# Optimization experiments

Measured on AMD Instinct MI355X. Metric: run time of the kernel, lower is better.

Reference implementation:

```python
import jax, jax.numpy as jnp
import numpy as np
from jax import lax

B, T, I, H, L = 64, 512, 256, 512, 2


def setup_inputs() -> dict:
    key = jax.random.key(0)
    ks = jax.random.split(key, 5)
    s_in = (6.0 / (H + I)) ** 0.5   # xavier-uniform-like scale
    s_hh = (6.0 / (H + H)) ** 0.5
    return {
        "x": jax.random.normal(ks[0], (B, T, I), jnp.float32),
        "h_0": jnp.zeros((L, B, H), jnp.float32),
        "W_ih_0": jax.random.normal(ks[1], (H, I), jnp.float32) * s_in,
        "W_hh_0": jax.random.normal(ks[2], (H, H), jnp.float32) * s_hh,
        "b_ih_0": jnp.zeros((H,), jnp.float32),
        "b_hh_0": jnp.zeros((H,), jnp.float32),
        "W_ih_1": jax.random.normal(ks[3], (H, H), jnp.float32) * s_hh,
        "W_hh_1": jax.random.normal(ks[4], (H, H), jnp.float32) * s_hh,
        "b_ih_1": jnp.zeros((H,), jnp.float32),
        "b_hh_1": jnp.zeros((H,), jnp.float32),
    }


def _rnn_layer(xs, h0, W_ih, W_hh, b_ih, b_hh):
    # Precompute the input-to-hidden projection for all timesteps at once
    # (same math as per-step F.linear, just batched): [B,T,H]
    xW = jnp.einsum('bti,hi->bth', xs, W_ih) + b_ih + b_hh

    def step(h, xw_t):  # h:[B,H], xw_t:[B,H]
        h_new = jnp.tanh(xw_t + h @ W_hh.T)
        return h_new, h_new

    h_last, ys = lax.scan(step, h0, jnp.swapaxes(xW, 0, 1))  # ys: [T,B,H]
    return jnp.swapaxes(ys, 0, 1), h_last


def reference(x, h_0, W_ih_0, W_hh_0, b_ih_0, b_hh_0,
              W_ih_1, W_hh_1, b_ih_1, b_hh_1):
    out0, h_n0 = _rnn_layer(x, h_0[0], W_ih_0, W_hh_0, b_ih_0, b_hh_0)
    out1, h_n1 = _rnn_layer(out0, h_0[1], W_ih_1, W_hh_1, b_ih_1, b_hh_1)
    h_n = jnp.stack([h_n0, h_n1], axis=0)  # [L,B,H]
    return out1, h_n
```

## Files before the change

kernel.cpp:

```cpp
#include <hip/hip_runtime.h>


#define kB 64
#define kT 512
#define kI 256
#define kH 512
#define kBH (kB * kH)

typedef _Float16 half8 __attribute__((ext_vector_type(8)));
typedef _Float16 half4v __attribute__((ext_vector_type(4)));
typedef float floatx4 __attribute__((ext_vector_type(4)));

constexpr size_t X16_B   = 0;
constexpr size_t OUT0M_B = 16u * 1024 * 1024;
constexpr size_t H1M_B   = OUT0M_B + (size_t)(kT + 1) * kBH * 2;
constexpr size_t CNT_B   = H1M_B + (size_t)(kT + 1) * kBH * 2;

__device__ inline half8 cvt8(const float* p) {
    const float4* p4 = (const float4*)p;
    float4 a = p4[0], b = p4[1];
    half8 h;
    h[0] = (_Float16)a.x; h[1] = (_Float16)a.y; h[2] = (_Float16)a.z; h[3] = (_Float16)a.w;
    h[4] = (_Float16)b.x; h[5] = (_Float16)b.y; h[6] = (_Float16)b.z; h[7] = (_Float16)b.w;
    return h;
}

__device__ inline void sc_store_half(_Float16* p, _Float16 v) {
    unsigned short u = __builtin_bit_cast(unsigned short, v);
    __hip_atomic_store((unsigned short*)p, u, __ATOMIC_RELAXED, __HIP_MEMORY_SCOPE_AGENT);
}

__device__ inline void wait_flag(const int* p, int target) {
    int guard = 0;
    while (__hip_atomic_load(p, __ATOMIC_RELAXED, __HIP_MEMORY_SCOPE_AGENT) < target) {
        if (++guard > 20000000) break;
    }
    asm volatile("" ::: "memory");
}

__device__ inline void publish(int* p, int lane) {
    asm volatile("" ::: "memory");
    __builtin_amdgcn_s_waitcnt(0x0F70);
    asm volatile("" ::: "memory");
    if (lane == 0)
        __hip_atomic_fetch_add(p, 1, __ATOMIC_RELAXED, __HIP_MEMORY_SCOPE_AGENT);
}

__global__ void cvt_x_kernel(const float* __restrict__ x, _Float16* __restrict__ x16) {
    size_t i = ((size_t)blockIdx.x * blockDim.x + threadIdx.x) * 4;
    size_t stride = (size_t)gridDim.x * blockDim.x * 4;
    const size_t n = (size_t)kB * kT * kI;
    for (; i < n; i += stride) {
        float4 v = *(const float4*)(x + i);
        half4v h;
        h[0] = (_Float16)v.x; h[1] = (_Float16)v.y; h[2] = (_Float16)v.z; h[3] = (_Float16)v.w;
        *(half4v*)(x16 + i) = h;
    }
}

__global__ void setup_kernel(const float* __restrict__ h0, _Float16* __restrict__ out0m,
                             _Float16* __restrict__ h1m, int* __restrict__ cnt) {
    int idx = blockIdx.x * blockDim.x + threadIdx.x;
    if (idx < kBH) out0m[idx] = (_Float16)h0[idx];
    else h1m[idx - kBH] = (_Float16)h0[idx];
    if (idx < 4096) cnt[idx] = 0;
}

__global__ __launch_bounds__(256, 1) void scan_kernel(
    const _Float16* __restrict__ x16, _Float16* __restrict__ out0m,
    _Float16* __restrict__ h1m, int* __restrict__ cnt0, int* __restrict__ cnt1,
    float* __restrict__ out1,
    const float* __restrict__ wih0, const float* __restrict__ whh0,
    const float* __restrict__ bih0, const float* __restrict__ bhh0,
    const float* __restrict__ wih1, const float* __restrict__ whh1,
    const float* __restrict__ bih1, const float* __restrict__ bhh1) {
    __shared__ float lds[2][4][256];

    const int blk = blockIdx.x;
    const int tid = threadIdx.x;
    const int wave = tid >> 6;
    const int lane = tid & 63;
    const int r = lane & 15;
    const int q = lane >> 4;
    const int layer = blk >> 7;
    const int lb = blk & 127;
    const int g = lb >> 5;
    const int ct = lb & 31;
    const int c0 = ct * 16;
    const int b0 = g * 16;

    const int col = lane & 15;
    const int row = wave * 4 + (lane >> 4);
    const int cc = c0 + col;
    const int bb = b0 + row;
    const int roff = (wave * 16 + col) * 4 + (lane >> 4);

    if (layer == 0) {
        half8 wfi[2], wfh[4];
#pragma unroll
        for (int m = 0; m < 2; ++m)
            wfi[m] = cvt8(wih0 + (size_t)(c0 + r) * kI + wave * 64 + m * 32 + q * 8);
#pragma unroll
        for (int m = 0; m < 4; ++m)
            wfh[m] = cvt8(whh0 + (size_t)(c0 + r) * kH + wave * 128 + m * 32 + q * 8);
        const float bias = bih0[cc] + bhh0[cc];
        int* flags = cnt0 + g * kT;

        for (int t = 0; t < kT; ++t) {
            const _Float16* xrow = x16 + ((size_t)(b0 + r) * kT + t) * kI + wave * 64 + q * 8;
            half8 xa0 = *(const half8*)(xrow);
            half8 xa1 = *(const half8*)(xrow + 32);
            floatx4 a0 = {0.f, 0.f, 0.f, 0.f};
            floatx4 a1 = {0.f, 0.f, 0.f, 0.f};
            a0 = __builtin_amdgcn_mfma_f32_16x16x32_f16(xa0, wfi[0], a0, 0, 0, 0);
            a1 = __builtin_amdgcn_mfma_f32_16x16x32_f16(xa1, wfi[1], a1, 0, 0, 0);

            if (t > 0) wait_flag(&flags[t - 1], 128);
            const _Float16* hrow = out0m + (size_t)t * kBH + (size_t)(b0 + r) * kH
                                   + wave * 128 + q * 8;
            half8 h0v = *(const half8*)(hrow);
            half8 h1v = *(const half8*)(hrow + 32);
            half8 h2v = *(const half8*)(hrow + 64);
            half8 h3v = *(const half8*)(hrow + 96);
            a0 = __builtin_amdgcn_mfma_f32_16x16x32_f16(h0v, wfh[0], a0, 0, 0, 0);
            a1 = __builtin_amdgcn_mfma_f32_16x16x32_f16(h1v, wfh[1], a1, 0, 0, 0);
            a0 = __builtin_amdgcn_mfma_f32_16x16x32_f16(h2v, wfh[2], a0, 0, 0, 0);
            a1 = __builtin_amdgcn_mfma_f32_16x16x32_f16(h3v, wfh[3], a1, 0, 0, 0);

            *(floatx4*)(&lds[t & 1][wave][lane * 4]) = a0 + a1;
            __syncthreads();
            const float* lp = &lds[t & 1][0][0];
            float s = lp[roff] + lp[256 + roff] + lp[512 + roff] + lp[768 + roff];
            float v = tanhf(s + bias);
            sc_store_half(out0m + (size_t)(t + 1) * kBH + (size_t)bb * kH + cc, (_Float16)v);
            publish(&flags[t], lane);
        }
    } else {
        half8 wfi[4], wfh[4];
#pragma unroll
        for (int m = 0; m < 4; ++m)
            wfi[m] = cvt8(wih1 + (size_t)(c0 + r) * kH + wave * 128 + m * 32 + q * 8);
#pragma unroll
        for (int m = 0; m < 4; ++m)
            wfh[m] = cvt8(whh1 + (size_t)(c0 + r) * kH + wave * 128 + m * 32 + q * 8);
        const float bias = bih1[cc] + bhh1[cc];
        int* flags0 = cnt0 + g * kT;
        int* flags1 = cnt1 + g * kT;

        for (int t = 0; t < kT; ++t) {
            floatx4 a0 = {0.f, 0.f, 0.f, 0.f};
            floatx4 a1 = {0.f, 0.f, 0.f, 0.f};
            wait_flag(&flags0[t], 128);
            const _Float16* irow = out0m + (size_t)(t + 1) * kBH + (size_t)(b0 + r) * kH
                                   + wave * 128 + q * 8;
            half8 i0 = *(const half8*)(irow);
            half8 i1 = *(const half8*)(irow + 32);
            half8 i2 = *(const half8*)(irow + 64);
            half8 i3 = *(const half8*)(irow + 96);
            a0 = __builtin_amdgcn_mfma_f32_16x16x32_f16(i0, wfi[0], a0, 0, 0, 0);
            a1 = __builtin_amdgcn_mfma_f32_16x16x32_f16(i1, wfi[1], a1, 0, 0, 0);
            a0 = __builtin_amdgcn_mfma_f32_16x16x32_f16(i2, wfi[2], a0, 0, 0, 0);
            a1 = __builtin_amdgcn_mfma_f32_16x16x32_f16(i3, wfi[3], a1, 0, 0, 0);
            if (t > 0) wait_flag(&flags1[t - 1], 128);
            const _Float16* hrow = h1m + (size_t)t * kBH + (size_t)(b0 + r) * kH
                                   + wave * 128 + q * 8;
            half8 h0v = *(const half8*)(hrow);
            half8 h1v = *(const half8*)(hrow + 32);
            half8 h2v = *(const half8*)(hrow + 64);
            half8 h3v = *(const half8*)(hrow + 96);
            a0 = __builtin_amdgcn_mfma_f32_16x16x32_f16(h0v, wfh[0], a0, 0, 0, 0);
            a1 = __builtin_amdgcn_mfma_f32_16x16x32_f16(h1v, wfh[1], a1, 0, 0, 0);
            a0 = __builtin_amdgcn_mfma_f32_16x16x32_f16(h2v, wfh[2], a0, 0, 0, 0);
            a1 = __builtin_amdgcn_mfma_f32_16x16x32_f16(h3v, wfh[3], a1, 0, 0, 0);

            *(floatx4*)(&lds[t & 1][wave][lane * 4]) = a0 + a1;
            __syncthreads();
            const float* lp = &lds[t & 1][0][0];
            float s = lp[roff] + lp[256 + roff] + lp[512 + roff] + lp[768 + roff];
            float v = tanhf(s + bias);
            out1[((size_t)bb * kT + t) * kH + cc] = v;
            sc_store_half(h1m + (size_t)(t + 1) * kBH + (size_t)bb * kH + cc, (_Float16)v);
            publish(&flags1[t], lane);
        }
    }
}

__global__ void finalize_kernel(const _Float16* __restrict__ out0m,
                                const _Float16* __restrict__ h1m,
                                float* __restrict__ out) {
    int idx = blockIdx.x * blockDim.x + threadIdx.x;
    float* hn = out + (size_t)kB * kT * kH;
    if (idx < kBH) hn[idx] = (float)out0m[(size_t)kT * kBH + idx];
    else hn[idx] = (float)h1m[(size_t)kT * kBH + (idx - kBH)];
}

extern "C" void kernel_launch(void* const* d_in, const int* in_sizes, int n_in,
                              void* d_out, int out_size, void* d_ws, size_t ws_size,
                              hipStream_t stream) {
    const float* x    = (const float*)d_in[0];
    const float* h0in = (const float*)d_in[1];
    const float* wih0 = (const float*)d_in[2];
    const float* whh0 = (const float*)d_in[3];
    const float* bih0 = (const float*)d_in[4];
    const float* bhh0 = (const float*)d_in[5];
    const float* wih1 = (const float*)d_in[6];
    const float* whh1 = (const float*)d_in[7];
    const float* bih1 = (const float*)d_in[8];
    const float* bhh1 = (const float*)d_in[9];
    float* out = (float*)d_out;
    char* ws = (char*)d_ws;

    _Float16* x16   = (_Float16*)(ws + X16_B);
    _Float16* out0m = (_Float16*)(ws + OUT0M_B);
    _Float16* h1m   = (_Float16*)(ws + H1M_B);
    int* cnt        = (int*)(ws + CNT_B);
    int* cnt0 = cnt;
    int* cnt1 = cnt + 4 * kT;

    cvt_x_kernel<<<1024, 256, 0, stream>>>(x, x16);
    setup_kernel<<<(2 * kBH) / 256, 256, 0, stream>>>(h0in, out0m, h1m, cnt);
    scan_kernel<<<256, 256, 0, stream>>>(x16, out0m, h1m, cnt0, cnt1, out,
                                         wih0, whh0, bih0, bhh0, wih1, whh1, bih1, bhh1);
    finalize_kernel<<<(2 * kBH) / 256, 256, 0, stream>>>(out0m, h1m, out);
}
```

Before: 2.182 ms.

## Replace per-step atomic counters with per-block slot stores and reorder layer-1 waits

Replaces the per-timestep shared atomic counter, which every wave incremented, with one slot per producer block. Each block writes its slot with a plain store of t+1 after a block barrier, and consumers poll all 32 slots in parallel with a wave vote. Layer 1 now does its recurrent h@W_hh MFMAs first and only then waits for layer 0's output. This lets it overlap with layer 0's progress. The aim is less atomic contention and a shorter critical-path latency per step, at the cost of an extra __syncthreads per step.

```diff
diff --git a/kernel.cpp b/kernel.cpp
--- a/kernel.cpp
+++ b/kernel.cpp
@@ -30,20 +30,23 @@
     __hip_atomic_store((unsigned short*)p, u, __ATOMIC_RELAXED, __HIP_MEMORY_SCOPE_AGENT);
 }
 
-__device__ inline void wait_flag(const int* p, int target) {
+__device__ inline void wait_slots(const int* slots, int target) {
+    const int* p = slots + (threadIdx.x & 31);
     int guard = 0;
-    while (__hip_atomic_load(p, __ATOMIC_RELAXED, __HIP_MEMORY_SCOPE_AGENT) < target) {
-        if (++guard > 20000000) break;
+    for (;;) {
+        int v = __hip_atomic_load(p, __ATOMIC_RELAXED, __HIP_MEMORY_SCOPE_AGENT);
+        if (__all(v >= target)) break;
+        if (++guard > 50000000) break;
     }
     asm volatile("" ::: "memory");
 }
 
-__device__ inline void publish(int* p, int lane) {
+__device__ inline void publish_block(int* slot, int t1, int tid) {
     asm volatile("" ::: "memory");
     __builtin_amdgcn_s_waitcnt(0x0F70);
-    asm volatile("" ::: "memory");
-    if (lane == 0)
-        __hip_atomic_fetch_add(p, 1, __ATOMIC_RELAXED, __HIP_MEMORY_SCOPE_AGENT);
+    __syncthreads();
+    if (tid == 0)
+        __hip_atomic_store(slot, t1, __ATOMIC_RELAXED, __HIP_MEMORY_SCOPE_AGENT);
 }
 
 __global__ void cvt_x_kernel(const float* __restrict__ x, _Float16* __restrict__ x16) {
@@ -63,12 +66,12 @@
     int idx = blockIdx.x * blockDim.x + threadIdx.x;
     if (idx < kBH) out0m[idx] = (_Float16)h0[idx];
     else h1m[idx - kBH] = (_Float16)h0[idx];
-    if (idx < 4096) cnt[idx] = 0;
+    if (idx < 256) cnt[idx] = 0;
 }
 
 __global__ __launch_bounds__(256, 1) void scan_kernel(
     const _Float16* __restrict__ x16, _Float16* __restrict__ out0m,
-    _Float16* __restrict__ h1m, int* __restrict__ cnt0, int* __restrict__ cnt1,
+    _Float16* __restrict__ h1m, int* __restrict__ slots0, int* __restrict__ slots1,
     float* __restrict__ out1,
     const float* __restrict__ wih0, const float* __restrict__ whh0,
     const float* __restrict__ bih0, const float* __restrict__ bhh0,
@@ -104,7 +107,7 @@
         for (int m = 0; m < 4; ++m)
             wfh[m] = cvt8(whh0 + (size_t)(c0 + r) * kH + wave * 128 + m * 32 + q * 8);
         const float bias = bih0[cc] + bhh0[cc];
-        int* flags = cnt0 + g * kT;
+        int* gslots = slots0 + g * 32;
 
         for (int t = 0; t < kT; ++t) {
             const _Float16* xrow = x16 + ((size_t)(b0 + r) * kT + t) * kI + wave * 64 + q * 8;
@@ -115,7 +118,7 @@
             a0 = __builtin_amdgcn_mfma_f32_16x16x32_f16(xa0, wfi[0], a0, 0, 0, 0);
             a1 = __builtin_amdgcn_mfma_f32_16x16x32_f16(xa1, wfi[1], a1, 0, 0, 0);
 
-            if (t > 0) wait_flag(&flags[t - 1], 128);
+            if (t > 0) wait_slots(gslots, t);
             const _Float16* hrow = out0m + (size_t)t * kBH + (size_t)(b0 + r) * kH
                                    + wave * 128 + q * 8;
             half8 h0v = *(const half8*)(hrow);
@@ -133,7 +136,7 @@
             float s = lp[roff] + lp[256 + roff] + lp[512 + roff] + lp[768 + roff];
             float v = tanhf(s + bias);
             sc_store_half(out0m + (size_t)(t + 1) * kBH + (size_t)bb * kH + cc, (_Float16)v);
-            publish(&flags[t], lane);
+            publish_block(&gslots[ct], t + 1, tid);
         }
     } else {
         half8 wfi[4], wfh[4];
@@ -144,13 +147,24 @@
         for (int m = 0; m < 4; ++m)
             wfh[m] = cvt8(whh1 + (size_t)(c0 + r) * kH + wave * 128 + m * 32 + q * 8);
         const float bias = bih1[cc] + bhh1[cc];
-        int* flags0 = cnt0 + g * kT;
-        int* flags1 = cnt1 + g * kT;
+        int* g0slots = slots0 + g * 32;
+        int* g1slots = slots1 + g * 32;
 
         for (int t = 0; t < kT; ++t) {
             floatx4 a0 = {0.f, 0.f, 0.f, 0.f};
             floatx4 a1 = {0.f, 0.f, 0.f, 0.f};
-            wait_flag(&flags0[t], 128);
+            if (t > 0) wait_slots(g1slots, t);
+            const _Float16* hrow = h1m + (size_t)t * kBH + (size_t)(b0 + r) * kH
+                                   + wave * 128 + q * 8;
+            half8 h0v = *(const half8*)(hrow);
+            half8 h1v = *(const half8*)(hrow + 32);
+            half8 h2v = *(const half8*)(hrow + 64);
+            half8 h3v = *(const half8*)(hrow + 96);
+            a0 = __builtin_amdgcn_mfma_f32_16x16x32_f16(h0v, wfh[0], a0, 0, 0, 0);
+            a1 = __builtin_amdgcn_mfma_f32_16x16x32_f16(h1v, wfh[1], a1, 0, 0, 0);
+            a0 = __builtin_amdgcn_mfma_f32_16x16x32_f16(h2v, wfh[2], a0, 0, 0, 0);
+            a1 = __builtin_amdgcn_mfma_f32_16x16x32_f16(h3v, wfh[3], a1, 0, 0, 0);
+            wait_slots(g0slots, t + 1);
             const _Float16* irow = out0m + (size_t)(t + 1) * kBH + (size_t)(b0 + r) * kH
                                    + wave * 128 + q * 8;
             half8 i0 = *(const half8*)(irow);
@@ -161,17 +175,6 @@
             a1 = __builtin_amdgcn_mfma_f32_16x16x32_f16(i1, wfi[1], a1, 0, 0, 0);
             a0 = __builtin_amdgcn_mfma_f32_16x16x32_f16(i2, wfi[2], a0, 0, 0, 0);
             a1 = __builtin_amdgcn_mfma_f32_16x16x32_f16(i3, wfi[3], a1, 0, 0, 0);
-            if (t > 0) wait_flag(&flags1[t - 1], 128);
-            const _Float16* hrow = h1m + (size_t)t * kBH + (size_t)(b0 + r) * kH
-                                   + wave * 128 + q * 8;
-            half8 h0v = *(const half8*)(hrow);
-            half8 h1v = *(const half8*)(hrow + 32);
-            half8 h2v = *(const half8*)(hrow + 64);
-            half8 h3v = *(const half8*)(hrow + 96);
-            a0 = __builtin_amdgcn_mfma_f32_16x16x32_f16(h0v, wfh[0], a0, 0, 0, 0);
-            a1 = __builtin_amdgcn_mfma_f32_16x16x32_f16(h1v, wfh[1], a1, 0, 0, 0);
-            a0 = __builtin_amdgcn_mfma_f32_16x16x32_f16(h2v, wfh[2], a0, 0, 0, 0);
-            a1 = __builtin_amdgcn_mfma_f32_16x16x32_f16(h3v, wfh[3], a1, 0, 0, 0);
 
             *(floatx4*)(&lds[t & 1][wave][lane * 4]) = a0 + a1;
             __syncthreads();
@@ -180,7 +183,7 @@
             float v = tanhf(s + bias);
             out1[((size_t)bb * kT + t) * kH + cc] = v;
             sc_store_half(h1m + (size_t)(t + 1) * kBH + (size_t)bb * kH + cc, (_Float16)v);
-            publish(&flags1[t], lane);
+            publish_block(&g1slots[ct], t + 1, tid);
         }
     }
 }
@@ -214,12 +217,12 @@
     _Float16* out0m = (_Float16*)(ws + OUT0M_B);
     _Float16* h1m   = (_Float16*)(ws + H1M_B);
     int* cnt        = (int*)(ws + CNT_B);
-    int* cnt0 = cnt;
-    int* cnt1 = cnt + 4 * kT;
+    int* slots0 = cnt;
+    int* slots1 = cnt + 128;
 
     cvt_x_kernel<<<1024, 256, 0, stream>>>(x, x16);
     setup_kernel<<<(2 * kBH) / 256, 256, 0, stream>>>(h0in, out0m, h1m, cnt);
-    scan_kernel<<<256, 256, 0, stream>>>(x16, out0m, h1m, cnt0, cnt1, out,
+    scan_kernel<<<256, 256, 0, stream>>>(x16, out0m, h1m, slots0, slots1, out,
                                          wih0, whh0, bih0, bhh0, wih1, whh1, bih1, bhh1);
     finalize_kernel<<<(2 * kBH) / 256, 256, 0, stream>>>(out0m, h1m, out);
 }
```

Result: faster. 2.097 ms (-3.9%).
